# Performance work log

Measured on AMD Instinct MI355X. Metric: run time of the kernel, lower is better.

The kernel has to match this reference:

```python
import jax, jax.numpy as jnp
import numpy as np

DEPTH = 4
HIDDEN = 256
ATOM_FDIM = 143
BOND_FDIM = 14
N_ATOMS = 65536
N_BONDS = 131072
MAX_NB = 6
ATOMS_PER_MOL = 32


def setup_inputs() -> dict:
    key = jax.random.key(0)
    ks = jax.random.split(key, 12)
    s = 0.05  # weight init scale
    return {
        'fatoms': jax.random.uniform(ks[0], (N_ATOMS, ATOM_FDIM), dtype=jnp.float32),
        'fbonds': jax.random.uniform(ks[1], (N_BONDS, ATOM_FDIM + BOND_FDIM), dtype=jnp.float32),
        'agraph': jax.random.randint(ks[2], (N_ATOMS, MAX_NB), 0, N_BONDS, dtype=jnp.int32),
        'bgraph': jax.random.randint(ks[3], (N_BONDS, MAX_NB), 0, N_BONDS, dtype=jnp.int32),
        'atoms_per_mol': ATOMS_PER_MOL,
        'W_i': jax.random.normal(ks[4], (ATOM_FDIM + BOND_FDIM, HIDDEN), dtype=jnp.float32) * s,
        'W_h': jax.random.normal(ks[5], (HIDDEN, HIDDEN), dtype=jnp.float32) * s,
        'W_o_w': jax.random.normal(ks[6], (ATOM_FDIM + HIDDEN, HIDDEN), dtype=jnp.float32) * s,
        'W_o_b': jax.random.normal(ks[7], (HIDDEN,), dtype=jnp.float32) * s,
        'W_a': jax.random.normal(ks[8], (HIDDEN, HIDDEN), dtype=jnp.float32) * s,
        'W_b_w': jax.random.normal(ks[9], (HIDDEN, HIDDEN), dtype=jnp.float32) * s,
        'W_b_b': jax.random.normal(ks[10], (HIDDEN,), dtype=jnp.float32) * s,
        'W_ma1': jax.random.normal(ks[11], (HIDDEN, 1), dtype=jnp.float32) * s,
    }


def reference(fatoms, fbonds, agraph, bgraph, atoms_per_mol,
              W_i, W_h, W_o_w, W_o_b, W_a, W_b_w, W_b_b, W_ma1):
    act = jax.nn.relu  # activation == 'ReLU'; dropout == 0 (identity)

    binput = fbonds @ W_i                      # [E, H]
    message = act(binput)
    for _ in range(DEPTH - 1):
        nei = message[bgraph]                  # [E, max_nb, H] gather
        # message attention over incoming messages (softmax over neighbor axis)
        att = jax.nn.softmax(nei @ W_ma1, axis=1)  # [E, max_nb, 1]
        nei = (nei * att).sum(axis=1)          # [E, H]
        message = act(binput + nei @ W_h)

    nei_a = message[agraph].sum(axis=1)        # [N, H]
    ainput = jnp.concatenate([fatoms, nei_a], axis=1)
    atom_h = act(ainput @ W_o_w + W_o_b)       # [N, H]

    # per-molecule self-attention pooling; equal-size molecules -> batched
    A = atoms_per_mol
    B = atom_h.shape[0] // A
    h = atom_h.reshape(B, A, HIDDEN)           # [B, A, H]
    scores = jnp.einsum('bad,bcd->bac', h @ W_a, h)   # [B, A, A]
    att_w = jax.nn.softmax(scores, axis=-1)
    att_h = act(jnp.einsum('bac,bcd->bad', att_w, h) @ W_b_w + W_b_b)
    mol_vecs = (h + att_h).sum(axis=1) / A     # [B, H]
    return mol_vecs
```

## Files before the change

### kernel.cpp

```cpp
#include <hip/hip_runtime.h>

typedef unsigned short u16;
typedef __attribute__((ext_vector_type(8))) short short8;
typedef __attribute__((ext_vector_type(4))) float floatx4;

__device__ __forceinline__ float bf2f(u16 u) {
    return __uint_as_float(((unsigned int)u) << 16);
}
__device__ __forceinline__ u16 f2bf(float f) {
    unsigned int i = __float_as_uint(f);
    unsigned int r = i + 0x7FFFu + ((i >> 16) & 1u);
    return (u16)(r >> 16);
}
__device__ __forceinline__ unsigned int relu2(unsigned int x) {
    unsigned int m = (((x >> 15) & 1u) * 0x0000FFFFu) | ((x >> 31) * 0xFFFF0000u);
    return x & ~m;
}

typedef __attribute__((address_space(3))) void lds_void;
typedef const __attribute__((address_space(1))) void g_void;
__device__ __forceinline__ void async_copy16(const void* g, void* l) {
    __builtin_amdgcn_global_load_lds((g_void*)g, (lds_void*)l, 16, 0, 0);
}

__device__ __forceinline__ void acc_bf8(float* a8, uint4 u, float wj) {
    a8[0] += wj * __uint_as_float(u.x << 16);
    a8[1] += wj * __uint_as_float(u.x & 0xffff0000u);
    a8[2] += wj * __uint_as_float(u.y << 16);
    a8[3] += wj * __uint_as_float(u.y & 0xffff0000u);
    a8[4] += wj * __uint_as_float(u.z << 16);
    a8[5] += wj * __uint_as_float(u.z & 0xffff0000u);
    a8[6] += wj * __uint_as_float(u.w << 16);
    a8[7] += wj * __uint_as_float(u.w & 0xffff0000u);
}

#define MFMA16(a, b, c) __builtin_amdgcn_mfma_f32_16x16x32_bf16(a, b, c, 0, 0, 0)

#define E_BONDS 131072
#define N_ATOMS_C 65536
#define KPAD_I 160
#define KPAD_O 416
#define N_MOLS 2048

__global__ __launch_bounds__(256) void prep_fbonds(const float* __restrict__ fb, u16* __restrict__ out) {
    int idx = blockIdx.x * 256 + threadIdx.x;
    int row = idx / KPAD_I;
    int col = idx - row * KPAD_I;
    float v = (col < 157) ? fb[(size_t)row * 157 + col] : 0.f;
    out[idx] = f2bf(v);
}

__global__ __launch_bounds__(256) void prep_wt(const float* __restrict__ W, u16* __restrict__ Wt, int K, int Kpad) {
    int idx = blockIdx.x * 256 + threadIdx.x;
    int n = idx / Kpad;
    int k = idx - n * Kpad;
    float v = (k < K) ? W[(size_t)k * 256 + n] : 0.f;
    Wt[idx] = f2bf(v);
}

__global__ __launch_bounds__(256) void prep_wo(const float* __restrict__ W, u16* __restrict__ Wt) {
    int idx = blockIdx.x * 256 + threadIdx.x;
    int n = idx / KPAD_O;
    int k = idx - n * KPAD_O;
    float v = 0.f;
    if (k < 256)      v = W[(size_t)(143 + k) * 256 + n];
    else if (k < 399) v = W[(size_t)(k - 256) * 256 + n];
    Wt[idx] = f2bf(v);
}

template <int EPI, bool RELUA>
__global__ __launch_bounds__(512, 3) void gemm256(
    const u16* __restrict__ A, const u16* __restrict__ Bt,
    u16* __restrict__ out,
    const float* __restrict__ bias, const float* __restrict__ wma,
    float* __restrict__ tout, int K)
{
    __shared__ char ldsbuf[33792];
    u16* Al = (u16*)ldsbuf;
    u16* Bl = (u16*)(ldsbuf + 8192);

    const int tid = threadIdx.x;
    const int w = tid >> 6, lane = tid & 63;
    const int quad = lane >> 4, mr = lane & 15;
    const int m0 = blockIdx.x * 128;

    floatx4 acc[16] = {};

    const u16* Ag = A + (size_t)(m0 + (tid & 127)) * K + ((tid >> 7) << 3);

    for (int k0 = 0; k0 < K; k0 += 32) {
        if (RELUA) {
            uint4 x = *(const uint4*)(Ag + k0);
            x.x = relu2(x.x); x.y = relu2(x.y); x.z = relu2(x.z); x.w = relu2(x.w);
            *(uint4*)(Al + tid * 8) = x;
        } else {
            async_copy16(Ag + k0, Al + tid * 8);
        }
#pragma unroll
        for (int i = 0; i < 2; ++i) {
            int c = tid + i * 512;
            async_copy16(Bt + (size_t)(c & 255) * K + k0 + ((c >> 8) << 3), Bl + c * 8);
        }
        __syncthreads();

        short8 af = *(const short8*)(Al + quad * 1024 + (w * 16 + mr) * 8);
#pragma unroll
        for (int j = 0; j < 16; ++j) {
            short8 bf = *(const short8*)(Bl + quad * 2048 + (j * 16 + mr) * 8);
            acc[j] = MFMA16(af, bf, acc[j]);
        }
        __syncthreads();
    }

    u16* slice = (u16*)ldsbuf + w * 2112;
    const int lhalf = lane >> 5;
    const int lcol = (lane & 31) * 8;
    float wmal8[8];
    if (EPI == 1) {
#pragma unroll
        for (int e = 0; e < 8; ++e) wmal8[e] = wma[lcol + e];
    }
    float bl16[16];
    if (EPI == 3) {
#pragma unroll
        for (int j = 0; j < 16; ++j) bl16[j] = bias[j * 16 + mr];
    }

#pragma unroll
    for (int p = 0; p < 2; ++p) {
        if ((quad >> 1) == p) {
            int lr = (quad & 1) * 4;
#pragma unroll
            for (int j = 0; j < 16; ++j)
#pragma unroll
                for (int r = 0; r < 4; ++r) {
                    float v = acc[j][r];
                    if (EPI == 3) { v += bl16[j]; v = v > 0.f ? v : 0.f; }
                    slice[(lr + r) * 264 + j * 16 + mr] = f2bf(v);
                }
        }
        __syncthreads();
#pragma unroll
        for (int round = 0; round < 4; ++round) {
            int rowl = round * 2 + lhalf;
            int row = m0 + w * 16 + p * 8 + rowl;
            size_t off = (size_t)row * 256 + lcol;
            short8 pv = *(const short8*)(slice + rowl * 264 + lcol);
            if (EPI == 0 || EPI == 3) {
                *(short8*)(out + off) = pv;
            } else {
                *(short8*)(out + off) = pv;
                float pdot = 0.f;
#pragma unroll
                for (int e = 0; e < 8; ++e) {
                    u16 u = (u16)pv[e];
                    u = (u & 0x8000u) ? (u16)0 : u;
                    pdot += bf2f(u) * wmal8[e];
                }
                pdot += __shfl_xor(pdot, 1); pdot += __shfl_xor(pdot, 2);
                pdot += __shfl_xor(pdot, 4); pdot += __shfl_xor(pdot, 8);
                pdot += __shfl_xor(pdot, 16);
                if ((lane & 31) == 0) tout[row] = pdot;
            }
        }
        __syncthreads();
    }
}

template <int MODE>
__global__ __launch_bounds__(512, 3) void fused_gg(
    const u16* src, const u16* __restrict__ Bt, const int* __restrict__ graph,
    const float* __restrict__ t_in, const u16* __restrict__ binput,
    const float* __restrict__ fatoms, const float* __restrict__ bias,
    const float* __restrict__ wma, u16* __restrict__ outp, float* __restrict__ t_out)
{
    constexpr int MT = (MODE == 2) ? 32 : 64;
    constexpr int KK = (MODE == 2) ? 416 : 256;
    constexpr int KP = KK + 8;
    constexpr int MF = MT / 16;
    constexpr int ABYT = MT * KP * 2;

    __shared__ __align__(16) char ldsbuf[64 * 264 * 2 + 16384];
    u16* As = (u16*)ldsbuf;
    u16* Bl = (u16*)(ldsbuf + ABYT);

    const int tid = threadIdx.x;
    const int w = tid >> 6, lane = tid & 63;
    const int quad = lane >> 4, mr = lane & 15;
    const int hw = tid >> 5, l32 = tid & 31;
    const int m0 = blockIdx.x * MT;

#pragma unroll
    for (int i = 0; i < 2; ++i) {
        int c = tid + i * 512;
        async_copy16(Bt + (size_t)(c & 255) * KK + ((c >> 8) << 3), Bl + c * 8);
    }

    for (int it = 0; it < MT / 16; ++it) {
        const int r = it * 16 + hw;
        const int e = m0 + r;
        const int* bg = graph + (size_t)e * 6;
        int2 b01 = *(const int2*)bg;
        int2 b23 = *(const int2*)(bg + 2);
        int2 b45 = *(const int2*)(bg + 4);
        int b[6] = {b01.x, b01.y, b23.x, b23.y, b45.x, b45.y};

        float wg[6];
        if (MODE != 2) {
            float s[6];
#pragma unroll
            for (int j = 0; j < 6; ++j) s[j] = t_in[b[j]];
            float mx = fmaxf(fmaxf(fmaxf(s[0], s[1]), fmaxf(s[2], s[3])), fmaxf(s[4], s[5]));
            float den = 0.f;
#pragma unroll
            for (int j = 0; j < 6; ++j) { wg[j] = __expf(s[j] - mx); den += wg[j]; }
            float inv = 1.f / den;
#pragma unroll
            for (int j = 0; j < 6; ++j) wg[j] *= inv;
        }

        float a8[8] = {};
#pragma unroll
        for (int j = 0; j < 6; ++j) {
            uint4 u = *(const uint4*)(src + (size_t)b[j] * 256 + l32 * 8);
            if (MODE == 1) { u.x = relu2(u.x); u.y = relu2(u.y); u.z = relu2(u.z); u.w = relu2(u.w); }
            acc_bf8(a8, u, (MODE == 2) ? 1.f : wg[j]);
        }
        short8 mv;
#pragma unroll
        for (int k = 0; k < 8; ++k) mv[k] = (short)f2bf(a8[k]);
        *(short8*)(As + r * KP + l32 * 8) = mv;

        if (MODE == 2) {
            const float* frow = fatoms + (size_t)e * 143;
#pragma unroll
            for (int i = 0; i < 5; ++i) {
                int c = l32 + i * 32;
                As[r * KP + 256 + c] = (c < 143) ? f2bf(frow[c]) : (u16)0;
            }
        }
    }

    floatx4 acc[MF][2] = {};

    for (int k0 = 0; k0 < KK; k0 += 32) {
        __syncthreads();
        short8 bf0 = *(const short8*)(Bl + quad * 2048 + ((w * 2 + 0) * 16 + mr) * 8);
        short8 bf1 = *(const short8*)(Bl + quad * 2048 + ((w * 2 + 1) * 16 + mr) * 8);
#pragma unroll
        for (int mf = 0; mf < MF; ++mf) {
            short8 af = *(const short8*)(As + (mf * 16 + mr) * KP + k0 + quad * 8);
            acc[mf][0] = MFMA16(af, bf0, acc[mf][0]);
            acc[mf][1] = MFMA16(af, bf1, acc[mf][1]);
        }
        __syncthreads();
        if (k0 + 32 < KK) {
#pragma unroll
            for (int i = 0; i < 2; ++i) {
                int c = tid + i * 512;
                async_copy16(Bt + (size_t)(c & 255) * KK + (k0 + 32) + ((c >> 8) << 3), Bl + c * 8);
            }
        }
    }

    if (MODE != 2) {
        float* Pf = (float*)ldsbuf;
        const int rrow = tid >> 4;
        const int rcol = (tid & 15) * 16;
        float wv[16];
#pragma unroll
        for (int e2 = 0; e2 < 16; ++e2) wv[e2] = wma[rcol + e2];

#pragma unroll
        for (int p = 0; p < 2; ++p) {
#pragma unroll
            for (int mi = 0; mi < 2; ++mi) {
#pragma unroll
                for (int jj = 0; jj < 2; ++jj)
#pragma unroll
                    for (int r = 0; r < 4; ++r)
                        Pf[(mi * 16 + quad * 4 + r) * 268 + (w * 2 + jj) * 16 + mr] = acc[p * 2 + mi][jj][r];
            }
            __syncthreads();
            const int grow = m0 + p * 32 + rrow;
            const u16* brow = binput + (size_t)grow * 256 + rcol;
            uint4 bu0 = *(const uint4*)brow;
            uint4 bu1 = *(const uint4*)(brow + 8);
            float bv[16] = {
                __uint_as_float(bu0.x << 16), __uint_as_float(bu0.x & 0xffff0000u),
                __uint_as_float(bu0.y << 16), __uint_as_float(bu0.y & 0xffff0000u),
                __uint_as_float(bu0.z << 16), __uint_as_float(bu0.z & 0xffff0000u),
                __uint_as_float(bu0.w << 16), __uint_as_float(bu0.w & 0xffff0000u),
                __uint_as_float(bu1.x << 16), __uint_as_float(bu1.x & 0xffff0000u),
                __uint_as_float(bu1.y << 16), __uint_as_float(bu1.y & 0xffff0000u),
                __uint_as_float(bu1.z << 16), __uint_as_float(bu1.z & 0xffff0000u),
                __uint_as_float(bu1.w << 16), __uint_as_float(bu1.w & 0xffff0000u)};
            const float* prow = Pf + rrow * 268 + rcol;
            float pdot = 0.f;
            short8 o0, o1;
#pragma unroll
            for (int e2 = 0; e2 < 16; ++e2) {
                float v = prow[e2] + bv[e2];
                v = v > 0.f ? v : 0.f;
                u16 q = f2bf(v);
                if (e2 < 8) o0[e2] = (short)q; else o1[e2 - 8] = (short)q;
                pdot += bf2f(q) * wv[e2];
            }
            size_t off = (size_t)grow * 256 + rcol;
            *(short8*)(outp + off) = o0;
            *(short8*)(outp + off + 8) = o1;
            pdot += __shfl_xor(pdot, 1); pdot += __shfl_xor(pdot, 2);
            pdot += __shfl_xor(pdot, 4); pdot += __shfl_xor(pdot, 8);
            if ((lane & 15) == 0) t_out[grow] = pdot;
            __syncthreads();
        }
    } else {
        u16* Pu = (u16*)ldsbuf;
        float bl0 = bias[(w * 2 + 0) * 16 + mr];
        float bl1 = bias[(w * 2 + 1) * 16 + mr];
#pragma unroll
        for (int mf = 0; mf < MF; ++mf)
#pragma unroll
            for (int r = 0; r < 4; ++r) {
                float v0 = acc[mf][0][r] + bl0; v0 = v0 > 0.f ? v0 : 0.f;
                float v1 = acc[mf][1][r] + bl1; v1 = v1 > 0.f ? v1 : 0.f;
                Pu[(mf * 16 + quad * 4 + r) * 264 + (w * 2 + 0) * 16 + mr] = f2bf(v0);
                Pu[(mf * 16 + quad * 4 + r) * 264 + (w * 2 + 1) * 16 + mr] = f2bf(v1);
            }
        __syncthreads();
        const int rrow = tid >> 4;
        const int rcol = (tid & 15) * 16;
        size_t off = (size_t)(m0 + rrow) * 256 + rcol;
        short8 v0 = *(const short8*)(Pu + rrow * 264 + rcol);
        short8 v1 = *(const short8*)(Pu + rrow * 264 + rcol + 8);
        *(short8*)(outp + off) = v0;
        *(short8*)(outp + off + 8) = v1;
    }
}

#define HSTR 260
__global__ __launch_bounds__(256) void mol_attn(const u16* __restrict__ atomh, const u16* __restrict__ hWg,
                                                u16* __restrict__ z) {
    __shared__ float hs[32 * HSTR];
    __shared__ float P[32 * 33];
    const int t = threadIdx.x;
    const int b = blockIdx.x;
    const u16* hbase = atomh + (size_t)b * 32 * 256;
    for (int e0 = t * 4; e0 < 8192; e0 += 1024) {
        int row = e0 >> 8, col = e0 & 255;
        ushort4 u = *(const ushort4*)(hbase + e0);
        floatx4 v; v.x = bf2f(u.x); v.y = bf2f(u.y); v.z = bf2f(u.z); v.w = bf2f(u.w);
        *(floatx4*)&hs[row * HSTR + col] = v;
    }
    __syncthreads();

    {
        int c = t & 31, a0 = t >> 5;
        const u16* hWb = hWg + (size_t)b * 32 * 256;
        for (int r = 0; r < 4; ++r) {
            int a = a0 + r * 8;
            const u16* hwrow = hWb + a * 256;
            float s = 0.f;
            for (int d = 0; d < 256; d += 4) {
                ushort4 u = *(const ushort4*)(hwrow + d);
                const float* hp = &hs[c * HSTR + d];
                s += bf2f(u.x) * hp[0] + bf2f(u.y) * hp[1] + bf2f(u.z) * hp[2] + bf2f(u.w) * hp[3];
            }
            P[a * 33 + c] = s;
        }
    }
    __syncthreads();
    if (t < 32) {
        float* prow = &P[t * 33];
        float mx = prow[0];
        for (int i = 1; i < 32; ++i) mx = fmaxf(mx, prow[i]);
        float den = 0.f;
        for (int i = 0; i < 32; ++i) { float ev = __expf(prow[i] - mx); prow[i] = ev; den += ev; }
        float inv = 1.f / den;
        for (int i = 0; i < 32; ++i) prow[i] *= inv;
    }
    __syncthreads();

    {
        int a = t >> 3, q = t & 7;
        floatx4 acc8[8];
#pragma unroll
        for (int i = 0; i < 8; ++i) acc8[i] = (floatx4){0.f, 0.f, 0.f, 0.f};
        const float* prow = &P[a * 33];
        for (int cc = 0; cc < 32; ++cc) {
            float p = prow[cc];
            const float* hrow = &hs[cc * HSTR + q * 4];
#pragma unroll
            for (int i = 0; i < 8; ++i) {
                floatx4 hv = *(const floatx4*)(hrow + i * 32);
                acc8[i] += p * hv;
            }
        }
        u16* zrow = z + ((size_t)b * 32 + a) * 256 + q * 4;
#pragma unroll
        for (int i = 0; i < 8; ++i) {
            ushort4 o;
            o.x = f2bf(acc8[i].x); o.y = f2bf(acc8[i].y); o.z = f2bf(acc8[i].z); o.w = f2bf(acc8[i].w);
            *(ushort4*)(zrow + i * 32) = o;
        }
    }
}

__global__ __launch_bounds__(256) void final_reduce(const u16* __restrict__ atomh, const u16* __restrict__ atth,
                                                    float* __restrict__ out) {
    int idx = blockIdx.x * 256 + threadIdx.x;
    int b = idx >> 8, d = idx & 255;
    const u16* ph = atomh + ((size_t)b * 32) * 256 + d;
    const u16* pa = atth + ((size_t)b * 32) * 256 + d;
    float s = 0.f;
#pragma unroll 4
    for (int a = 0; a < 32; ++a) s += bf2f(ph[a * 256]) + bf2f(pa[a * 256]);
    out[idx] = s * 0.03125f;
}

#define O_FBP      ((size_t)0)
#define O_BINPUT   ((size_t)41943040)
#define O_MSGA     ((size_t)109051904)
#define O_MSGB     ((size_t)176160768)
#define O_W        ((size_t)243269632)
#define O_WTI      (O_W)
#define O_WTH      (O_W + 81920)
#define O_WTO      (O_W + 212992)
#define O_WTA      (O_W + 425984)
#define O_WTB      (O_W + 557056)
#define WS_NEED    ((size_t)243957760)

extern "C" void kernel_launch(void* const* d_in, const int* in_sizes, int n_in,
                              void* d_out, int out_size, void* d_ws, size_t ws_size,
                              hipStream_t stream) {
    const float* fatoms = (const float*)d_in[0];
    const float* fbonds = (const float*)d_in[1];
    const int*   agraph = (const int*)d_in[2];
    const int*   bgraph = (const int*)d_in[3];
    const float* W_i    = (const float*)d_in[5];
    const float* W_h    = (const float*)d_in[6];
    const float* W_o_w  = (const float*)d_in[7];
    const float* W_o_b  = (const float*)d_in[8];
    const float* W_a    = (const float*)d_in[9];
    const float* W_b_w  = (const float*)d_in[10];
    const float* W_b_b  = (const float*)d_in[11];
    const float* W_ma1  = (const float*)d_in[12];
    float* out = (float*)d_out;

    if (ws_size < WS_NEED) return;

    char* ws = (char*)d_ws;
    u16* fbp     = (u16*)(ws + O_FBP);
    u16* binput  = (u16*)(ws + O_BINPUT);
    u16* msgA    = (u16*)(ws + O_MSGA);
    u16* msgB    = (u16*)(ws + O_MSGB);
    u16* wti     = (u16*)(ws + O_WTI);
    u16* wth     = (u16*)(ws + O_WTH);
    u16* wto     = (u16*)(ws + O_WTO);
    u16* wta     = (u16*)(ws + O_WTA);
    u16* wtb     = (u16*)(ws + O_WTB);
    u16* atomh   = (u16*)(ws + O_FBP);
    u16* hW      = (u16*)(ws + O_BINPUT);
    u16* zbuf    = (u16*)(ws + O_BINPUT + 33554432);
    u16* atth    = (u16*)(ws + O_MSGA);
    float* tA = (float*)d_out;
    float* tB = tA + E_BONDS;

    prep_fbonds<<<81920, 256, 0, stream>>>(fbonds, fbp);
    prep_wt<<<160, 256, 0, stream>>>(W_i, wti, 157, KPAD_I);
    prep_wt<<<256, 256, 0, stream>>>(W_h, wth, 256, 256);
    prep_wo<<<416, 256, 0, stream>>>(W_o_w, wto);
    prep_wt<<<256, 256, 0, stream>>>(W_a, wta, 256, 256);
    prep_wt<<<256, 256, 0, stream>>>(W_b_w, wtb, 256, 256);

    gemm256<1, false><<<1024, 512, 0, stream>>>(fbp, wti, binput, nullptr, W_ma1, tA, KPAD_I);

    fused_gg<1><<<E_BONDS / 64, 512, 0, stream>>>(binput, wth, bgraph, tA, binput, nullptr, nullptr, W_ma1, msgA, tB);
    fused_gg<0><<<E_BONDS / 64, 512, 0, stream>>>(msgA,   wth, bgraph, tB, binput, nullptr, nullptr, W_ma1, msgB, tA);
    fused_gg<0><<<E_BONDS / 64, 512, 0, stream>>>(msgB,   wth, bgraph, tA, binput, nullptr, nullptr, W_ma1, msgA, tB);

    fused_gg<2><<<N_ATOMS_C / 32, 512, 0, stream>>>(msgA, wto, agraph, nullptr, nullptr, fatoms, W_o_b, nullptr, atomh, nullptr);

    gemm256<0, false><<<512, 512, 0, stream>>>(atomh, wta, hW, nullptr, nullptr, nullptr, 256);
    mol_attn<<<N_MOLS, 256, 0, stream>>>(atomh, hW, zbuf);
    gemm256<3, false><<<512, 512, 0, stream>>>(zbuf, wtb, atth, W_b_b, nullptr, nullptr, 256);

    final_reduce<<<N_MOLS, 256, 0, stream>>>(atomh, atth, out);
}
```

Measured before the change: 748.5 us.

## Read W tiles straight from global and double fused_gg block to 1024 threads

Result: no change. 753.8 us (+0.7%).

```diff
diff --git a/kernel.cpp b/kernel.cpp
--- a/kernel.cpp
+++ b/kernel.cpp
@@ -168,7 +168,7 @@
 }
 
 template <int MODE>
-__global__ __launch_bounds__(512, 3) void fused_gg(
+__global__ __launch_bounds__(1024, 8) void fused_gg(
     const u16* src, const u16* __restrict__ Bt, const int* __restrict__ graph,
     const float* __restrict__ t_in, const u16* __restrict__ binput,
     const float* __restrict__ fatoms, const float* __restrict__ bias,
@@ -178,11 +178,10 @@
     constexpr int KK = (MODE == 2) ? 416 : 256;
     constexpr int KP = KK + 8;
     constexpr int MF = MT / 16;
-    constexpr int ABYT = MT * KP * 2;
-
-    __shared__ __align__(16) char ldsbuf[64 * 264 * 2 + 16384];
+    constexpr int LDSB = (MODE == 2) ? (32 * 424 * 2) : (32 * 268 * 4);
+
+    __shared__ __align__(16) char ldsbuf[LDSB];
     u16* As = (u16*)ldsbuf;
-    u16* Bl = (u16*)(ldsbuf + ABYT);
 
     const int tid = threadIdx.x;
     const int w = tid >> 6, lane = tid & 63;
@@ -191,13 +190,8 @@
     const int m0 = blockIdx.x * MT;
 
 #pragma unroll
-    for (int i = 0; i < 2; ++i) {
-        int c = tid + i * 512;
-        async_copy16(Bt + (size_t)(c & 255) * KK + ((c >> 8) << 3), Bl + c * 8);
-    }
-
-    for (int it = 0; it < MT / 16; ++it) {
-        const int r = it * 16 + hw;
+    for (int it = 0; it < MT / 32; ++it) {
+        const int r = it * 32 + hw;
         const int e = m0 + r;
         const int* bg = graph + (size_t)e * 6;
         int2 b01 = *(const int2*)bg;
@@ -240,101 +234,80 @@
             }
         }
     }
-
-    floatx4 acc[MF][2] = {};
-
-    for (int k0 = 0; k0 < KK; k0 += 32) {
-        __syncthreads();
-        short8 bf0 = *(const short8*)(Bl + quad * 2048 + ((w * 2 + 0) * 16 + mr) * 8);
-        short8 bf1 = *(const short8*)(Bl + quad * 2048 + ((w * 2 + 1) * 16 + mr) * 8);
+    __syncthreads();
+
+    floatx4 acc[MF] = {};
+    const u16* bp = Bt + (size_t)(w * 16 + mr) * KK + quad * 8;
+#pragma unroll 2
+    for (int ks = 0; ks < KK / 32; ++ks) {
+        const int k0 = ks * 32;
+        short8 bf = *(const short8*)(bp + k0);
 #pragma unroll
         for (int mf = 0; mf < MF; ++mf) {
             short8 af = *(const short8*)(As + (mf * 16 + mr) * KP + k0 + quad * 8);
-            acc[mf][0] = MFMA16(af, bf0, acc[mf][0]);
-            acc[mf][1] = MFMA16(af, bf1, acc[mf][1]);
-        }
-        __syncthreads();
-        if (k0 + 32 < KK) {
-#pragma unroll
-            for (int i = 0; i < 2; ++i) {
-                int c = tid + i * 512;
-                async_copy16(Bt + (size_t)(c & 255) * KK + (k0 + 32) + ((c >> 8) << 3), Bl + c * 8);
-            }
-        }
-    }
+            acc[mf] = MFMA16(af, bf, acc[mf]);
+        }
+    }
+    __syncthreads();
 
     if (MODE != 2) {
         float* Pf = (float*)ldsbuf;
-        const int rrow = tid >> 4;
-        const int rcol = (tid & 15) * 16;
-        float wv[16];
-#pragma unroll
-        for (int e2 = 0; e2 < 16; ++e2) wv[e2] = wma[rcol + e2];
+        const int rrow = tid >> 5;
+        const int rcol = l32 * 8;
+        float wv[8];
+#pragma unroll
+        for (int e2 = 0; e2 < 8; ++e2) wv[e2] = wma[rcol + e2];
 
 #pragma unroll
         for (int p = 0; p < 2; ++p) {
 #pragma unroll
-            for (int mi = 0; mi < 2; ++mi) {
-#pragma unroll
-                for (int jj = 0; jj < 2; ++jj)
-#pragma unroll
-                    for (int r = 0; r < 4; ++r)
-                        Pf[(mi * 16 + quad * 4 + r) * 268 + (w * 2 + jj) * 16 + mr] = acc[p * 2 + mi][jj][r];
-            }
+            for (int mi = 0; mi < 2; ++mi)
+#pragma unroll
+                for (int r = 0; r < 4; ++r)
+                    Pf[(mi * 16 + quad * 4 + r) * 268 + w * 16 + mr] = acc[p * 2 + mi][r];
             __syncthreads();
             const int grow = m0 + p * 32 + rrow;
             const u16* brow = binput + (size_t)grow * 256 + rcol;
-            uint4 bu0 = *(const uint4*)brow;
-            uint4 bu1 = *(const uint4*)(brow + 8);
-            float bv[16] = {
-                __uint_as_float(bu0.x << 16), __uint_as_float(bu0.x & 0xffff0000u),
-                __uint_as_float(bu0.y << 16), __uint_as_float(bu0.y & 0xffff0000u),
-                __uint_as_float(bu0.z << 16), __uint_as_float(bu0.z & 0xffff0000u),
-                __uint_as_float(bu0.w << 16), __uint_as_float(bu0.w & 0xffff0000u),
-                __uint_as_float(bu1.x << 16), __uint_as_float(bu1.x & 0xffff0000u),
-                __uint_as_float(bu1.y << 16), __uint_as_float(bu1.y & 0xffff0000u),
-                __uint_as_float(bu1.z << 16), __uint_as_float(bu1.z & 0xffff0000u),
-                __uint_as_float(bu1.w << 16), __uint_as_float(bu1.w & 0xffff0000u)};
+            uint4 bu = *(const uint4*)brow;
+            float bv[8] = {
+                __uint_as_float(bu.x << 16), __uint_as_float(bu.x & 0xffff0000u),
+                __uint_as_float(bu.y << 16), __uint_as_float(bu.y & 0xffff0000u),
+                __uint_as_float(bu.z << 16), __uint_as_float(bu.z & 0xffff0000u),
+                __uint_as_float(bu.w << 16), __uint_as_float(bu.w & 0xffff0000u)};
             const float* prow = Pf + rrow * 268 + rcol;
             float pdot = 0.f;
-            short8 o0, o1;
-#pragma unroll
-            for (int e2 = 0; e2 < 16; ++e2) {
+            short8 o;
+#pragma unroll
+            for (int e2 = 0; e2 < 8; ++e2) {
                 float v = prow[e2] + bv[e2];
                 v = v > 0.f ? v : 0.f;
                 u16 q = f2bf(v);
-                if (e2 < 8) o0[e2] = (short)q; else o1[e2 - 8] = (short)q;
+                o[e2] = (short)q;
                 pdot += bf2f(q) * wv[e2];
             }
-            size_t off = (size_t)grow * 256 + rcol;
-            *(short8*)(outp + off) = o0;
-            *(short8*)(outp + off + 8) = o1;
+            *(short8*)(outp + (size_t)grow * 256 + rcol) = o;
             pdot += __shfl_xor(pdot, 1); pdot += __shfl_xor(pdot, 2);
             pdot += __shfl_xor(pdot, 4); pdot += __shfl_xor(pdot, 8);
-            if ((lane & 15) == 0) t_out[grow] = pdot;
+            pdot += __shfl_xor(pdot, 16);
+            if (l32 == 0) t_out[grow] = pdot;
             __syncthreads();
         }
     } else {
         u16* Pu = (u16*)ldsbuf;
-        float bl0 = bias[(w * 2 + 0) * 16 + mr];
-        float bl1 = bias[(w * 2 + 1) * 16 + mr];
+        float bl = bias[w * 16 + mr];
 #pragma unroll
         for (int mf = 0; mf < MF; ++mf)
 #pragma unroll
             for (int r = 0; r < 4; ++r) {
-                float v0 = acc[mf][0][r] + bl0; v0 = v0 > 0.f ? v0 : 0.f;
-                float v1 = acc[mf][1][r] + bl1; v1 = v1 > 0.f ? v1 : 0.f;
-                Pu[(mf * 16 + quad * 4 + r) * 264 + (w * 2 + 0) * 16 + mr] = f2bf(v0);
-                Pu[(mf * 16 + quad * 4 + r) * 264 + (w * 2 + 1) * 16 + mr] = f2bf(v1);
+                float v = acc[mf][r] + bl;
+                v = v > 0.f ? v : 0.f;
+                Pu[(mf * 16 + quad * 4 + r) * 264 + w * 16 + mr] = f2bf(v);
             }
         __syncthreads();
-        const int rrow = tid >> 4;
-        const int rcol = (tid & 15) * 16;
+        const int rrow = tid >> 5;
+        const int rcol = l32 * 8;
         size_t off = (size_t)(m0 + rrow) * 256 + rcol;
-        short8 v0 = *(const short8*)(Pu + rrow * 264 + rcol);
-        short8 v1 = *(const short8*)(Pu + rrow * 264 + rcol + 8);
-        *(short8*)(outp + off) = v0;
-        *(short8*)(outp + off + 8) = v1;
+        *(short8*)(outp + off) = *(const short8*)(Pu + rrow * 264 + rcol);
     }
 }
 
@@ -475,11 +448,11 @@
 
     gemm256<1, false><<<1024, 512, 0, stream>>>(fbp, wti, binput, nullptr, W_ma1, tA, KPAD_I);
 
-    fused_gg<1><<<E_BONDS / 64, 512, 0, stream>>>(binput, wth, bgraph, tA, binput, nullptr, nullptr, W_ma1, msgA, tB);
-    fused_gg<0><<<E_BONDS / 64, 512, 0, stream>>>(msgA,   wth, bgraph, tB, binput, nullptr, nullptr, W_ma1, msgB, tA);
-    fused_gg<0><<<E_BONDS / 64, 512, 0, stream>>>(msgB,   wth, bgraph, tA, binput, nullptr, nullptr, W_ma1, msgA, tB);
-
-    fused_gg<2><<<N_ATOMS_C / 32, 512, 0, stream>>>(msgA, wto, agraph, nullptr, nullptr, fatoms, W_o_b, nullptr, atomh, nullptr);
+    fused_gg<1><<<E_BONDS / 64, 1024, 0, stream>>>(binput, wth, bgraph, tA, binput, nullptr, nullptr, W_ma1, msgA, tB);
+    fused_gg<0><<<E_BONDS / 64, 1024, 0, stream>>>(msgA,   wth, bgraph, tB, binput, nullptr, nullptr, W_ma1, msgB, tA);
+    fused_gg<0><<<E_BONDS / 64, 1024, 0, stream>>>(msgB,   wth, bgraph, tA, binput, nullptr, nullptr, W_ma1, msgA, tB);
+
+    fused_gg<2><<<N_ATOMS_C / 32, 1024, 0, stream>>>(msgA, wto, agraph, nullptr, nullptr, fatoms, W_o_b, nullptr, atomh, nullptr);
 
     gemm256<0, false><<<512, 512, 0, stream>>>(atomh, wta, hW, nullptr, nullptr, nullptr, 256);
     mol_attn<<<N_MOLS, 256, 0, stream>>>(atomh, hW, zbuf);
```
